# Optimization experiments

Hardware: AMD Instinct MI355X
Metric: run time of the kernel (lower is better)

## Reference

```python
import jax, jax.numpy as jnp
import numpy as np

K = 3       # kernel_size
STRIDE = 1
PAD = 1


def conv3d(x, w, b):
    # standard Conv3d NCDHW, used to predict per-tap offsets
    y = jax.lax.conv_general_dilated(
        x, w, window_strides=(STRIDE,) * 3, padding=[(PAD, PAD)] * 3,
        dimension_numbers=("NCDHW", "OIDHW", "NCDHW"))
    return y + b[None, :, None, None, None]


def trilinear_sample(xn, pd, ph, pw):
    # xn: (C,D,H,W); pd/ph/pw: (T,Do,Ho,Wo) float voxel coords.
    # Trilinear interpolation with zeros padding (grid_sample semantics).
    C, D, H, W = xn.shape
    d0 = jnp.floor(pd); h0 = jnp.floor(ph); w0 = jnp.floor(pw)
    fd = pd - d0; fh = ph - h0; fw = pw - w0
    d0 = d0.astype(jnp.int32); h0 = h0.astype(jnp.int32); w0 = w0.astype(jnp.int32)
    out = jnp.zeros((C,) + pd.shape, xn.dtype)
    for dd in (0, 1):
        wd = fd if dd else 1.0 - fd
        di = d0 + dd
        for hh in (0, 1):
            wh = fh if hh else 1.0 - fh
            hi = h0 + hh
            for ww in (0, 1):
                wc = fw if ww else 1.0 - fw
                wi = w0 + ww
                valid = (di >= 0) & (di < D) & (hi >= 0) & (hi < H) & (wi >= 0) & (wi < W)
                wgt = jnp.where(valid, wd * wh * wc, 0.0)
                g = xn[:, jnp.clip(di, 0, D - 1), jnp.clip(hi, 0, H - 1), jnp.clip(wi, 0, W - 1)]
                out = out + wgt[None] * g
    return out  # (C,T,Do,Ho,Wo)


def deform_conv3d(x, offset, weight):
    # x: (N,C,D,H,W); offset: (N,3*K^3,Do,Ho,Wo); weight: (O,C,K,K,K)
    N, C, D, H, W = x.shape
    Do = (D + 2 * PAD - K) // STRIDE + 1
    Ho = (H + 2 * PAD - K) // STRIDE + 1
    Wo = (W + 2 * PAD - K) // STRIDE + 1
    T = K ** 3
    kd, kh, kw = jnp.meshgrid(jnp.arange(K), jnp.arange(K), jnp.arange(K), indexing="ij")
    kd = kd.reshape(T, 1, 1, 1).astype(x.dtype)
    kh = kh.reshape(T, 1, 1, 1).astype(x.dtype)
    kw = kw.reshape(T, 1, 1, 1).astype(x.dtype)
    base_d = kd - PAD + (jnp.arange(Do, dtype=x.dtype) * STRIDE).reshape(1, Do, 1, 1)
    base_h = kh - PAD + (jnp.arange(Ho, dtype=x.dtype) * STRIDE).reshape(1, 1, Ho, 1)
    base_w = kw - PAD + (jnp.arange(Wo, dtype=x.dtype) * STRIDE).reshape(1, 1, 1, Wo)
    off = offset.reshape(N, 3, T, Do, Ho, Wo)  # matches offset.view(N,3,K,K,K,...) tap ordering
    pd = base_d[None] + off[:, 0]
    ph = base_h[None] + off[:, 1]
    pw = base_w[None] + off[:, 2]
    sampled = jax.vmap(trilinear_sample)(x, pd, ph, pw)  # (N,C,T,Do,Ho,Wo)
    O = weight.shape[0]
    w2 = weight.reshape(O, C, T)
    return jnp.einsum("nctdhw,oct->nodhw", sampled, w2)


def setup_inputs() -> dict:
    key = jax.random.key(0)
    k1, k2, k3 = jax.random.split(key, 3)
    N, C, O, S = 2, 16, 32, 48
    x = jax.random.normal(k1, (N, C, S, S, S), jnp.float32)
    fan_in = C * K ** 3
    weight = jax.random.normal(k2, (O, C, K, K, K), jnp.float32) * (1.0 / np.sqrt(fan_in))
    # offset conv params; small scale so sampled positions stay near the base grid
    offset_w = jax.random.normal(k3, (3 * K ** 3, C, K, K, K), jnp.float32) * 0.02
    offset_b = jnp.zeros((3 * K ** 3,), jnp.float32)
    return {"x": x, "weight": weight, "offset_w": offset_w, "offset_b": offset_b}


def reference(x, weight, offset_w, offset_b):
    offset = conv3d(x, offset_w, offset_b)
    return deform_conv3d(x, offset, weight)
```

## Files before the change

kernel.cpp:

```cpp
#include <hip/hip_runtime.h>
#include <hip/hip_bf16.h>

#define SDIM 48
#define SP   110592
#define C_IN 16
#define O_OUT 32
#define T27  27
#define G81  81

typedef __attribute__((ext_vector_type(8))) short bf16x8;
typedef __attribute__((ext_vector_type(4))) float f32x4;
typedef __attribute__((ext_vector_type(2))) float f32x2;

__device__ __forceinline__ float bf2f(unsigned short u) {
    unsigned int x = ((unsigned int)u) << 16;
    return __builtin_bit_cast(float, x);
}
__device__ __forceinline__ unsigned short f2bf(float f) {
    unsigned int x = __builtin_bit_cast(unsigned int, f);
    x += 0x7fffu + ((x >> 16) & 1u);
    return (unsigned short)(x >> 16);
}

__global__ __launch_bounds__(256)
void prep_xT(const float* __restrict__ x, unsigned short* __restrict__ xT) {
    __shared__ float l[256 * 17];
    const int tid = threadIdx.x;
    const int b   = blockIdx.x;
    const int n   = b / 432;
    const int sp0 = (b - n * 432) * 256;
    #pragma unroll
    for (int c = 0; c < 16; ++c)
        l[tid * 17 + c] = x[((size_t)(n * 16 + c)) * SP + sp0 + tid];
    __syncthreads();
    unsigned int u[8];
    #pragma unroll
    for (int q = 0; q < 8; ++q) {
        unsigned short a = f2bf(l[tid * 17 + 2 * q]);
        unsigned short bb = f2bf(l[tid * 17 + 2 * q + 1]);
        u[q] = (unsigned int)a | ((unsigned int)bb << 16);
    }
    uint4* dst = (uint4*)(xT + ((size_t)(n * SP + sp0 + tid)) * 16);
    dst[0] = make_uint4(u[0], u[1], u[2], u[3]);
    dst[1] = make_uint4(u[4], u[5], u[6], u[7]);
}

__global__ __launch_bounds__(256)
void prep_bfrag(const float* __restrict__ ow, unsigned short* __restrict__ Bf) {
    int idx = blockIdx.x * 256 + threadIdx.x;
    int r    = idx & 7;
    int lane = (idx >> 3) & 63;
    int snt  = idx >> 9;
    int s = snt / 6, nt = snt - s * 6;
    int kk  = ((lane >> 4) << 3) + r;
    int g   = nt * 16 + (lane & 15);
    int tap = 2 * s + (kk >> 4);
    int c   = kk & 15;
    float v = 0.f;
    if (tap < 27 && g < 81) v = ow[((size_t)(g * 16 + c)) * 27 + tap];
    Bf[idx] = f2bf(v);
}

__global__ __launch_bounds__(256)
void prep_wfrag(const float* __restrict__ w, unsigned short* __restrict__ Wf) {
    int idx = blockIdx.x * 256 + threadIdx.x;
    int r    = idx & 7;
    int lane = (idx >> 3) & 63;
    int snt  = idx >> 9;
    int s = snt >> 1, nt = snt & 1;
    int kk  = ((lane >> 4) << 3) + r;
    int o   = nt * 16 + (lane & 15);
    int tap = 2 * s + (kk >> 4);
    int c   = kk & 15;
    float v = 0.f;
    if (tap < 27) v = w[((size_t)(o * 16 + c)) * 27 + tap];
    Wf[idx] = f2bf(v);
}

__global__ __launch_bounds__(256)
void offs_conv_mfma(const unsigned short* __restrict__ xT,
                    const unsigned short* __restrict__ Bf,
                    const float* __restrict__ ob,
                    unsigned short* __restrict__ offs) {
    __shared__ unsigned short Alds[256 * 8];
    const int tid  = threadIdx.x;
    const int lane = tid & 63;
    const int wid  = tid >> 6;
    const int j    = wid;
    const int m    = tid & 63;
    const int gm   = blockIdx.x * 64 + m;
    const int n    = (gm >= SP) ? 1 : 0;
    const int sp   = gm - n * SP;
    const int z    = sp / 2304;
    const int rem  = sp - z * 2304;
    const int y    = rem / 48;
    const int xx   = rem - y * 48;
    const int tapoff = j >> 1;
    const int half   = j & 1;

    auto stage_load = [&](int s) -> uint4 {
        int tap = 2 * s + tapoff;
        int kd = tap / 9;
        int t2 = tap - kd * 9;
        int kh = t2 / 3;
        int kw = t2 - kh * 3;
        int di = z + kd - 1, hi = y + kh - 1, wi = xx + kw - 1;
        bool ok = (tap < 27) && ((unsigned)di < 48u) && ((unsigned)hi < 48u) &&
                  ((unsigned)wi < 48u);
        uint4 v = make_uint4(0u, 0u, 0u, 0u);
        if (ok) {
            size_t off = ((size_t)(n * SP + (di * 2304 + hi * 48 + wi))) * 16 + half * 8;
            v = *(const uint4*)(xT + off);
        }
        return v;
    };

    f32x4 acc[6];
    #pragma unroll
    for (int t = 0; t < 6; ++t) acc[t] = (f32x4){0.f, 0.f, 0.f, 0.f};

    uint4 v = stage_load(0);
    for (int s = 0; s < 14; ++s) {
        __syncthreads();
        *(uint4*)&Alds[tid * 8] = v;
        __syncthreads();
        if (s < 13) v = stage_load(s + 1);
        bf16x8 a = *(const bf16x8*)&Alds[(((lane >> 4) * 64) + (wid * 16) + (lane & 15)) * 8];
        const bf16x8* bp = (const bf16x8*)Bf + (size_t)(s * 6) * 64 + lane;
        #pragma unroll
        for (int nt = 0; nt < 6; ++nt) {
            bf16x8 b = bp[nt * 64];
            acc[nt] = __builtin_amdgcn_mfma_f32_16x16x32_bf16(a, b, acc[nt], 0, 0, 0);
        }
    }

    const int mrow = wid * 16 + ((lane >> 4) << 2);
    const int gmr  = blockIdx.x * 64 + mrow;
    const int n2   = (gmr >= SP) ? 1 : 0;
    const int spr  = gmr - n2 * SP;
    #pragma unroll
    for (int nt = 0; nt < 6; ++nt) {
        int g = nt * 16 + (lane & 15);
        if (g < 81) {
            float bia = ob[g];
            unsigned short h0 = f2bf(acc[nt][0] + bia);
            unsigned short h1 = f2bf(acc[nt][1] + bia);
            unsigned short h2 = f2bf(acc[nt][2] + bia);
            unsigned short h3 = f2bf(acc[nt][3] + bia);
            uint2 pv;
            pv.x = (unsigned int)h0 | ((unsigned int)h1 << 16);
            pv.y = (unsigned int)h2 | ((unsigned int)h3 << 16);
            *(uint2*)(offs + ((size_t)(n2 * 81 + g)) * SP + spr) = pv;
        }
    }
}

__global__ __launch_bounds__(448, 7)
void deform_fused(const unsigned short* __restrict__ xT,
                  const unsigned short* __restrict__ Wf,
                  const unsigned short* __restrict__ offs,
                  float* __restrict__ out) {
    __shared__ __align__(16) unsigned char smem[17920];
    unsigned short* S  = (unsigned short*)smem;
    float*          Cp = (float*)smem;

    const int tid  = threadIdx.x;
    const int lane = tid & 63;
    const int wv   = tid >> 6;
    const int p    = tid & 15;
    const int t    = tid >> 4;
    const int n    = (blockIdx.x >= 6912) ? 1 : 0;
    const int sp0  = blockIdx.x * 16 - n * SP;
    const int sp   = sp0 + p;
    const int z    = sp / 2304;
    const int rm   = sp - z * 2304;
    const int y    = rm / 48;
    const int xx   = rm - y * 48;

    const unsigned short* offn = offs + (size_t)n * G81 * SP + sp;
    const uint4* xq4 = (const uint4*)(xT + (size_t)n * SP * 16);

    uint4 ra = make_uint4(0u, 0u, 0u, 0u);
    uint4 rb = make_uint4(0u, 0u, 0u, 0u);
    if (t < 27) {
        const int kd = t / 9;
        const int t2 = t - kd * 9;
        const int kh = t2 / 3;
        const int kw = t2 - kh * 3;
        float pd = (float)(z + kd - 1)  + bf2f(offn[(size_t)t * SP]);
        float ph = (float)(y + kh - 1)  + bf2f(offn[(size_t)(27 + t) * SP]);
        float pw = (float)(xx + kw - 1) + bf2f(offn[(size_t)(54 + t) * SP]);
        float df = floorf(pd), hf = floorf(ph), wf = floorf(pw);
        float fd = pd - df, fh = ph - hf, fw = pw - wf;
        int d0 = (int)df, h0 = (int)hf, w0 = (int)wf;
        float wd0 = ((unsigned)d0       < 48u) ? (1.f - fd) : 0.f;
        float wd1 = ((unsigned)(d0 + 1) < 48u) ? fd : 0.f;
        float wh0 = ((unsigned)h0       < 48u) ? (1.f - fh) : 0.f;
        float wh1 = ((unsigned)(h0 + 1) < 48u) ? fh : 0.f;
        float ww0 = ((unsigned)w0       < 48u) ? (1.f - fw) : 0.f;
        float ww1 = ((unsigned)(w0 + 1) < 48u) ? fw : 0.f;
        int dc0 = min(max(d0,     0), 47) * 2304;
        int dc1 = min(max(d0 + 1, 0), 47) * 2304;
        int hc0 = min(max(h0,     0), 47) * 48;
        int hc1 = min(max(h0 + 1, 0), 47) * 48;
        int wc0 = min(max(w0,     0), 47);
        int wc1 = min(max(w0 + 1, 0), 47);

        float wdh[4] = {wd0 * wh0, wd0 * wh1, wd1 * wh0, wd1 * wh1};
        int   rdh[4] = {dc0 + hc0, dc0 + hc1, dc1 + hc0, dc1 + hc1};

        f32x2 s2v[8];
        #pragma unroll
        for (int q = 0; q < 8; ++q) s2v[q] = (f32x2){0.f, 0.f};

        #pragma unroll
        for (int g2 = 0; g2 < 2; ++g2) {
            uint4 cv[8];
            float cwt[4];
            #pragma unroll
            for (int pidx = 0; pidx < 2; ++pidx) {
                int jj = g2 * 2 + pidx;
                int i0 = rdh[jj] + wc0;
                int i1 = rdh[jj] + wc1;
                cv[pidx * 4 + 0] = xq4[(size_t)i0 * 2];
                cv[pidx * 4 + 1] = xq4[(size_t)i0 * 2 + 1];
                cv[pidx * 4 + 2] = xq4[(size_t)i1 * 2];
                cv[pidx * 4 + 3] = xq4[(size_t)i1 * 2 + 1];
                cwt[pidx * 2 + 0] = wdh[jj] * ww0;
                cwt[pidx * 2 + 1] = wdh[jj] * ww1;
            }
            #pragma unroll
            for (int pidx = 0; pidx < 2; ++pidx) {
                #pragma unroll
                for (int wsel = 0; wsel < 2; ++wsel) {
                    f32x2 w2;
                    w2.x = cwt[pidx * 2 + wsel];
                    w2.y = w2.x;
                    const uint4& lo4 = cv[pidx * 4 + wsel * 2];
                    const uint4& hi4 = cv[pidx * 4 + wsel * 2 + 1];
                    unsigned int wd_[8] = {lo4.x, lo4.y, lo4.z, lo4.w,
                                           hi4.x, hi4.y, hi4.z, hi4.w};
                    #pragma unroll
                    for (int q = 0; q < 8; ++q) {
                        f32x2 xv;
                        xv.x = __builtin_bit_cast(float, wd_[q] << 16);
                        xv.y = __builtin_bit_cast(float, wd_[q] & 0xffff0000u);
                        s2v[q] = __builtin_elementwise_fma(xv, w2, s2v[q]);
                    }
                }
            }
        }
        unsigned int o_[8];
        #pragma unroll
        for (int q = 0; q < 8; ++q) {
            unsigned int r_;
            asm("v_cvt_pk_bf16_f32 %0, %1, %2" : "=v"(r_) : "v"(s2v[q].x), "v"(s2v[q].y));
            o_[q] = r_;
        }
        ra = make_uint4(o_[0], o_[1], o_[2], o_[3]);
        rb = make_uint4(o_[4], o_[5], o_[6], o_[7]);
    }
    {
        unsigned short* wp_ = S + p * 488 + t * 16;
        *(uint4*)wp_       = ra;
        *(uint4*)(wp_ + 8) = rb;
    }
    __syncthreads();

    f32x4 acc0 = (f32x4){0.f, 0.f, 0.f, 0.f};
    f32x4 acc1 = (f32x4){0.f, 0.f, 0.f, 0.f};
    {
        const int q   = lane >> 4;
        const int pr  = lane & 15;
        const int ks0 = 2 * wv;
        bf16x8 a0 = *(const bf16x8*)(S + pr * 488 + ks0 * 32 + q * 8);
        bf16x8 a1 = *(const bf16x8*)(S + pr * 488 + (ks0 + 1) * 32 + q * 8);
        const bf16x8* bp0 = (const bf16x8*)Wf + (size_t)((ks0 + 0) * 2) * 64 + lane;
        const bf16x8* bp1 = (const bf16x8*)Wf + (size_t)((ks0 + 1) * 2) * 64 + lane;
        acc0 = __builtin_amdgcn_mfma_f32_16x16x32_bf16(a0, bp0[0],  acc0, 0, 0, 0);
        acc1 = __builtin_amdgcn_mfma_f32_16x16x32_bf16(a0, bp0[64], acc1, 0, 0, 0);
        acc0 = __builtin_amdgcn_mfma_f32_16x16x32_bf16(a1, bp1[0],  acc0, 0, 0, 0);
        acc1 = __builtin_amdgcn_mfma_f32_16x16x32_bf16(a1, bp1[64], acc1, 0, 0, 0);
    }
    __syncthreads();

    {
        const int o16 = lane & 15;
        const int m0  = (lane >> 4) << 2;
        *(f32x4*)&Cp[(wv * 32 + o16)      * 20 + m0] = acc0;
        *(f32x4*)&Cp[(wv * 32 + 16 + o16) * 20 + m0] = acc1;
    }
    __syncthreads();

    #pragma unroll
    for (int rep = 0; rep < 2; ++rep) {
        int idx = tid + rep * 448;
        if (rep == 0 || tid < 64) {
            int o = idx >> 4;
            int m = idx & 15;
            float r0 = 0.f;
            #pragma unroll
            for (int w2 = 0; w2 < 7; ++w2)
                r0 += Cp[(w2 * 32 + o) * 20 + m];
            out[((size_t)(n * O_OUT + o)) * SP + sp0 + m] = r0;
        }
    }
}

extern "C" void kernel_launch(void* const* d_in, const int* in_sizes, int n_in,
                              void* d_out, int out_size, void* d_ws, size_t ws_size,
                              hipStream_t stream) {
    (void)in_sizes; (void)n_in; (void)out_size; (void)ws_size;
    const float* x      = (const float*)d_in[0];
    const float* weight = (const float*)d_in[1];
    const float* ow     = (const float*)d_in[2];
    const float* ob     = (const float*)d_in[3];
    float* out = (float*)d_out;

    unsigned short* offs_b = (unsigned short*)d_ws;
    unsigned short* xT     = offs_b + (size_t)2 * 81 * SP;
    unsigned short* Bf     = xT + (size_t)2 * SP * 16;
    unsigned short* Wf     = Bf + 43008;

    prep_xT<<<864, 256, 0, stream>>>(x, xT);
    prep_bfrag<<<168, 256, 0, stream>>>(ow, Bf);
    prep_wfrag<<<56, 256, 0, stream>>>(weight, Wf);
    offs_conv_mfma<<<3456, 256, 0, stream>>>(xT, Bf, ob, offs_b);
    deform_fused<<<13824, 448, 0, stream>>>(xT, Wf, offs_b, out);
}
```

Measured before the change: 170.0 us.

## Store offsets position-major with padded stride, swizzle block order, relax occupancy

The offset conv now transposes its MFMA results through LDS and writes offsets in a position-major layout (96 bf16 per voxel) using 16-byte coalesced stores. The deform kernel then reads each voxel's 81 offsets from one contiguous row instead of from 81 planes strided by the spatial size. Both kernels remap blockIdx with an 8-way interleave, which changes the order in which blocks are scheduled. The deform kernel's launch-bounds minimum occupancy drops from 7 to 4, giving the compiler more registers per thread. The cost is extra LDS, an added barrier in the offset kernel and a larger padded offset buffer.

```diff
diff --git a/kernel.cpp b/kernel.cpp
--- a/kernel.cpp
+++ b/kernel.cpp
@@ -6,7 +6,7 @@
 #define C_IN 16
 #define O_OUT 32
 #define T27  27
-#define G81  81
+#define OST  96
 
 typedef __attribute__((ext_vector_type(8))) short bf16x8;
 typedef __attribute__((ext_vector_type(4))) float f32x4;
@@ -83,20 +83,20 @@
                     const float* __restrict__ ob,
                     unsigned short* __restrict__ offs) {
     __shared__ unsigned short Alds[256 * 8];
+    __shared__ unsigned short Tl[64 * 104];
     const int tid  = threadIdx.x;
     const int lane = tid & 63;
     const int wid  = tid >> 6;
-    const int j    = wid;
+    const int bid  = (blockIdx.x & 7) * 432 + (blockIdx.x >> 3);
     const int m    = tid & 63;
-    const int gm   = blockIdx.x * 64 + m;
-    const int n    = (gm >= SP) ? 1 : 0;
-    const int sp   = gm - n * SP;
+    const int n    = (bid >= 1728) ? 1 : 0;
+    const int sp   = bid * 64 + m - n * SP;
     const int z    = sp / 2304;
     const int rem  = sp - z * 2304;
     const int y    = rem / 48;
     const int xx   = rem - y * 48;
-    const int tapoff = j >> 1;
-    const int half   = j & 1;
+    const int tapoff = wid >> 1;
+    const int half   = wid & 1;
 
     auto stage_load = [&](int s) -> uint4 {
         int tap = 2 * s + tapoff;
@@ -135,27 +135,27 @@
     }
 
     const int mrow = wid * 16 + ((lane >> 4) << 2);
-    const int gmr  = blockIdx.x * 64 + mrow;
-    const int n2   = (gmr >= SP) ? 1 : 0;
-    const int spr  = gmr - n2 * SP;
     #pragma unroll
     for (int nt = 0; nt < 6; ++nt) {
         int g = nt * 16 + (lane & 15);
-        if (g < 81) {
-            float bia = ob[g];
-            unsigned short h0 = f2bf(acc[nt][0] + bia);
-            unsigned short h1 = f2bf(acc[nt][1] + bia);
-            unsigned short h2 = f2bf(acc[nt][2] + bia);
-            unsigned short h3 = f2bf(acc[nt][3] + bia);
-            uint2 pv;
-            pv.x = (unsigned int)h0 | ((unsigned int)h1 << 16);
-            pv.y = (unsigned int)h2 | ((unsigned int)h3 << 16);
-            *(uint2*)(offs + ((size_t)(n2 * 81 + g)) * SP + spr) = pv;
-        }
-    }
-}
-
-__global__ __launch_bounds__(448, 7)
+        float bia = (g < 81) ? ob[g] : 0.f;
+        #pragma unroll
+        for (int r = 0; r < 4; ++r)
+            Tl[(mrow + r) * 104 + g] = f2bf(acc[nt][r] + bia);
+    }
+    __syncthreads();
+    unsigned short* dst = offs + (size_t)bid * (64 * OST);
+    #pragma unroll
+    for (int k = 0; k < 3; ++k) {
+        int idx = k * 256 + tid;
+        int row = idx / 12;
+        int col = (idx - row * 12) * 8;
+        uint4 vv = *(const uint4*)&Tl[row * 104 + col];
+        *(uint4*)(dst + row * OST + col) = vv;
+    }
+}
+
+__global__ __launch_bounds__(448, 4)
 void deform_fused(const unsigned short* __restrict__ xT,
                   const unsigned short* __restrict__ Wf,
                   const unsigned short* __restrict__ offs,
@@ -169,15 +169,16 @@
     const int wv   = tid >> 6;
     const int p    = tid & 15;
     const int t    = tid >> 4;
-    const int n    = (blockIdx.x >= 6912) ? 1 : 0;
-    const int sp0  = blockIdx.x * 16 - n * SP;
+    const int bid  = (blockIdx.x & 7) * 1728 + (blockIdx.x >> 3);
+    const int n    = (bid >= 6912) ? 1 : 0;
+    const int sp0  = bid * 16 - n * SP;
     const int sp   = sp0 + p;
     const int z    = sp / 2304;
     const int rm   = sp - z * 2304;
     const int y    = rm / 48;
     const int xx   = rm - y * 48;
 
-    const unsigned short* offn = offs + (size_t)n * G81 * SP + sp;
+    const unsigned short* offr = offs + ((size_t)(n * SP + sp)) * OST;
     const uint4* xq4 = (const uint4*)(xT + (size_t)n * SP * 16);
 
     uint4 ra = make_uint4(0u, 0u, 0u, 0u);
@@ -187,9 +188,9 @@
         const int t2 = t - kd * 9;
         const int kh = t2 / 3;
         const int kw = t2 - kh * 3;
-        float pd = (float)(z + kd - 1)  + bf2f(offn[(size_t)t * SP]);
-        float ph = (float)(y + kh - 1)  + bf2f(offn[(size_t)(27 + t) * SP]);
-        float pw = (float)(xx + kw - 1) + bf2f(offn[(size_t)(54 + t) * SP]);
+        float pd = (float)(z + kd - 1)  + bf2f(offr[t]);
+        float ph = (float)(y + kh - 1)  + bf2f(offr[27 + t]);
+        float pw = (float)(xx + kw - 1) + bf2f(offr[54 + t]);
         float df = floorf(pd), hf = floorf(ph), wf = floorf(pw);
         float fd = pd - df, fh = ph - hf, fw = pw - wf;
         int d0 = (int)df, h0 = (int)hf, w0 = (int)wf;
@@ -318,7 +319,7 @@
     float* out = (float*)d_out;
 
     unsigned short* offs_b = (unsigned short*)d_ws;
-    unsigned short* xT     = offs_b + (size_t)2 * 81 * SP;
+    unsigned short* xT     = offs_b + (size_t)2 * SP * OST;
     unsigned short* Bf     = xT + (size_t)2 * SP * 16;
     unsigned short* Wf     = Bf + 43008;
 
```

Measured after the change: 184.5 us. +8.6%, slower.
